# Kernel tuning notes

Hardware: AMD Instinct MI355X
Metric: run time of the kernel (lower is better)

## Reference

```python
import jax, jax.numpy as jnp
import numpy as np

NUM_CLASSES = 40
EOS_COEF = 0.1
IGNORE = 255
W_CLASS, W_MASK, W_DICE = 2.0, 5.0, 5.0
EPS = 1e-8


def setup_inputs() -> dict:
    key = jax.random.key(0)
    k1, k2, k3, k4 = jax.random.split(key, 4)
    B, Q, H, W = 4, 100, 256, 256
    pred_logits = jax.random.normal(k1, (B, Q, NUM_CLASSES + 1), dtype=jnp.float32)
    pred_masks = jax.random.normal(k2, (B, Q, H, W), dtype=jnp.float32)
    targets = jax.random.randint(k3, (B, H, W), 0, NUM_CLASSES)
    ign = jax.random.uniform(k4, (B, H, W)) < 0.05
    targets = jnp.where(ign, IGNORE, targets).astype(jnp.int32)
    return {"pred_logits": pred_logits, "pred_masks": pred_masks, "targets": targets}


def reference(pred_logits, pred_masks, targets):
    B, Q, _ = pred_logits.shape
    C = NUM_CLASSES
    f32 = jnp.float32
    valid = targets != IGNORE                      # [B,H,W]
    tgt_safe = jnp.where(valid, targets, 0)        # in-range for indexing

    # ---- loss_labels: pixel->query assignment, per-query mode label ----
    # sigmoid is monotone, so argmax over queries of raw logits == argmax of sigmoid
    assign = jnp.argmax(pred_masks, axis=1)        # [B,H,W]
    b_idx = jnp.broadcast_to(jnp.arange(B)[:, None, None], targets.shape)
    # counts[b,q,c] = #valid pixels assigned to query q with label c
    counts = jnp.zeros((B, Q, C), f32).at[b_idx, assign, tgt_safe].add(valid.astype(f32))
    has_pix = counts.sum(-1) > 0                   # [B,Q]
    # mode = argmax of counts (ties -> smallest class, matching torch.mode)
    target_classes = jnp.where(has_pix, jnp.argmax(counts, axis=-1), C)  # [B,Q]

    logp = jax.nn.log_softmax(pred_logits, axis=-1)                      # [B,Q,C+1]
    nll = -jnp.take_along_axis(logp, target_classes[..., None], axis=-1)[..., 0]
    empty_weight = jnp.ones(C + 1, f32).at[-1].set(EOS_COEF)
    # ignore_index = num_classes in the CE over classes
    ce = jnp.where(target_classes != C, nll * empty_weight[target_classes], 0.0)
    p = jnp.exp(-ce)
    loss_ce = jnp.mean((1.0 - p) ** 2 * ce)

    # ---- loss_masks: per-pixel CE over queries + per-class dice ----
    logp_pix = jax.nn.log_softmax(pred_masks, axis=1)                    # [B,Q,H,W]
    nll_pix = -jnp.take_along_axis(logp_pix, tgt_safe[:, None], axis=1)[:, 0]  # [B,H,W]
    n_valid = valid.astype(f32).sum()
    ce_mask = jnp.sum(jnp.where(valid, nll_pix, 0.0)) / jnp.maximum(n_valid, 1.0)

    sig = jax.nn.sigmoid(pred_masks)                                     # [B,Q,H,W]
    tmask = (targets[:, None] == jnp.arange(C)[None, :, None, None]).astype(f32)  # [B,C,H,W]
    vm = valid[:, None].astype(f32)                                      # [B,1,H,W]
    inter = jnp.einsum('bqhw,bchw->bqc', sig, tmask * vm)                # numerator uses valid mask
    src_sum = sig.sum(axis=(2, 3))                                       # [B,Q]
    tsum = tmask.sum(axis=(2, 3))                                        # [B,C]
    dice = 2.0 * inter / (src_sum[:, :, None] + tsum[:, None, :] + EPS)  # [B,Q,C]
    present = tsum.sum(axis=0) > 0                                       # [C]
    dice_loss = jnp.sum(jnp.where(present, 1.0 - dice.mean(axis=(0, 1)), 0.0)) / C

    combined = W_MASK * ce_mask + W_DICE * dice_loss
    return W_CLASS * loss_ce + combined
```

## Files before the change

kernel.cpp:

```cpp
#include <hip/hip_runtime.h>
#include <hip/hip_bf16.h>

constexpr int B = 4, Q = 100, C = 40, Cp1 = 41, HW = 65536;
constexpr int NPIX = B * HW;
constexpr int CHUNKS = 4;
constexpr int CPX = HW / CHUNKS;

constexpr int WS_WORDS = 32562;

__global__ void kZ(unsigned* __restrict__ ws, int n) {
    int i = blockIdx.x * blockDim.x + threadIdx.x;
    for (; i < n; i += gridDim.x * blockDim.x) ws[i] = 0u;
}

__global__ __launch_bounds__(256) void kA(const float* __restrict__ masks,
                                          const int* __restrict__ targets,
                                          unsigned* __restrict__ counts,
                                          unsigned* __restrict__ tsum,
                                          float* __restrict__ ce_sum,
                                          unsigned* __restrict__ n_valid) {
    int tid = threadIdx.x;
    int pix = blockIdx.x * 256 + tid;
    int b = pix >> 16;
    int hw = pix & 65535;
    const float* mp = masks + (size_t)b * Q * HW + hw;
    int tgt = targets[pix];

    float m = -INFINITY, s = 0.f, xt = 0.f;
    int amax = 0;
    #pragma unroll 4
    for (int q = 0; q < Q; ++q) {
        float v = mp[(size_t)q * HW];
        float nm = fmaxf(m, v);
        s = s * __expf(m - nm) + __expf(v - nm);
        amax = (v > m) ? q : amax;
        m = nm;
        xt = (q == tgt) ? v : xt;
    }

    __shared__ unsigned ts_local[C];
    __shared__ float cred[4];
    __shared__ unsigned vred[4];
    if (tid < C) ts_local[tid] = 0u;
    __syncthreads();

    float ce = 0.f;
    unsigned nv = 0;
    if (tgt != 255) {
        float lse = m + __logf(s);
        ce = lse - xt;
        nv = 1;
        atomicAdd(&counts[((size_t)b * Q + amax) * C + tgt], 1u);
        atomicAdd(&ts_local[tgt], 1u);
    }

    for (int off = 32; off; off >>= 1) {
        ce += __shfl_xor(ce, off);
        nv += __shfl_xor(nv, off);
    }
    int lane = tid & 63, wave = tid >> 6;
    if (lane == 0) { cred[wave] = ce; vred[wave] = nv; }
    __syncthreads();
    if (tid == 0) {
        atomicAdd(ce_sum, cred[0] + cred[1] + cred[2] + cred[3]);
        atomicAdd(n_valid, vred[0] + vred[1] + vred[2] + vred[3]);
    }
    if (tid < C) {
        unsigned t = ts_local[tid];
        if (t) atomicAdd(&tsum[b * C + tid], t);
    }
}

__global__ __launch_bounds__(256) void kB(const float* __restrict__ masks,
                                          const int* __restrict__ targets,
                                          float* __restrict__ inter,
                                          float* __restrict__ src_sum) {
    __shared__ float hist[C][256];
    int tid = threadIdx.x;
    int bq = blockIdx.x >> 2;
    int chunk = blockIdx.x & 3;
    int b = bq / Q;
    const float* mp = masks + (size_t)bq * HW + chunk * CPX;
    const int* tp = targets + (size_t)b * HW + chunk * CPX;

    #pragma unroll
    for (int c = 0; c < C; ++c) hist[c][tid] = 0.f;

    float sacc = 0.f;
    for (int it = 0; it < CPX / 1024; ++it) {
        int off = it * 1024 + tid * 4;
        float4 x = *(const float4*)(mp + off);
        int4 tg = *(const int4*)(tp + off);
        float xs[4] = {x.x, x.y, x.z, x.w};
        int cs[4] = {tg.x, tg.y, tg.z, tg.w};
        #pragma unroll
        for (int j = 0; j < 4; ++j) {
            float sig = 1.f / (1.f + __expf(-xs[j]));
            sacc += sig;
            if ((unsigned)cs[j] < (unsigned)C) hist[cs[j]][tid] += sig;
        }
    }

    for (int off = 32; off; off >>= 1) sacc += __shfl_xor(sacc, off);
    int lane = tid & 63, wave = tid >> 6;
    if (lane == 0) atomicAdd(&src_sum[bq], sacc);

    __syncthreads();
    for (int c = wave * 10; c < wave * 10 + 10; ++c) {
        float h = hist[c][lane] + hist[c][lane + 64] + hist[c][lane + 128] + hist[c][lane + 192];
        for (int off = 32; off; off >>= 1) h += __shfl_xor(h, off);
        if (lane == 0) atomicAdd(&inter[(size_t)bq * C + c], h);
    }
}

__global__ __launch_bounds__(512) void kC(const float* __restrict__ logits,
                                          const unsigned* __restrict__ counts,
                                          const unsigned* __restrict__ tsum,
                                          const float* __restrict__ inter,
                                          const float* __restrict__ src_sum,
                                          const float* __restrict__ ce_sum,
                                          const unsigned* __restrict__ n_valid,
                                          float* __restrict__ out) {
    int tid = threadIdx.x;
    __shared__ float dice_sum[C];
    __shared__ float wred[8];
    __shared__ float s_lce;
    if (tid < C) dice_sum[tid] = 0.f;

    float ce_acc = 0.f;
    for (int i = tid; i < B * Q; i += 512) {
        const unsigned* cnt = counts + (size_t)i * C;
        unsigned best = 0;
        int tc = C;
        #pragma unroll
        for (int c = 0; c < C; ++c) {
            unsigned v = cnt[c];
            if (v > best) { best = v; tc = c; }
        }
        if (tc != C) {
            const float* lg = logits + (size_t)i * Cp1;
            float mm = -INFINITY, xt = 0.f;
            #pragma unroll
            for (int c = 0; c < Cp1; ++c) {
                float v = lg[c];
                mm = fmaxf(mm, v);
                if (c == tc) xt = v;
            }
            float ss = 0.f;
            #pragma unroll
            for (int c = 0; c < Cp1; ++c) ss += __expf(lg[c] - mm);
            float nll = mm + __logf(ss) - xt;
            float p = __expf(-nll);
            float om = 1.f - p;
            ce_acc += om * om * nll;
        }
    }
    for (int off = 32; off; off >>= 1) ce_acc += __shfl_xor(ce_acc, off);
    if ((tid & 63) == 0) wred[tid >> 6] = ce_acc;
    __syncthreads();
    if (tid == 0) {
        float t = 0.f;
        for (int w = 0; w < 8; ++w) t += wred[w];
        s_lce = t;
    }

    for (int i = tid; i < B * Q * C; i += 512) {
        int bq = i / C, c = i - bq * C;
        float denom = src_sum[bq] + (float)tsum[(bq / Q) * C + c] + 1e-8f;
        atomicAdd(&dice_sum[c], 2.f * inter[i] / denom);
    }
    __syncthreads();

    if (tid == 0) {
        float dl = 0.f;
        for (int c = 0; c < C; ++c) {
            unsigned ts = tsum[c] + tsum[C + c] + tsum[2 * C + c] + tsum[3 * C + c];
            if (ts > 0) dl += 1.f - dice_sum[c] * (1.f / (B * Q));
        }
        dl *= (1.f / C);
        float ce_mask = ce_sum[0] / fmaxf((float)n_valid[0], 1.f);
        float lce = s_lce * (1.f / (B * Q));
        out[0] = 2.f * lce + 5.f * ce_mask + 5.f * dl;
    }
}

extern "C" void kernel_launch(void* const* d_in, const int* in_sizes, int n_in,
                              void* d_out, int out_size, void* d_ws, size_t ws_size,
                              hipStream_t stream) {
    const float* logits  = (const float*)d_in[0];
    const float* masks   = (const float*)d_in[1];
    const int*   targets = (const int*)d_in[2];
    float* out = (float*)d_out;

    unsigned* ws      = (unsigned*)d_ws;
    unsigned* counts  = ws;
    unsigned* tsum    = ws + 16000;
    float*    inter   = (float*)(ws + 16160);
    float*    src_sum = (float*)(ws + 32160);
    float*    ce_sum  = (float*)(ws + 32560);
    unsigned* n_valid = ws + 32561;

    kZ<<<32, 256, 0, stream>>>(ws, WS_WORDS);
    kA<<<NPIX / 256, 256, 0, stream>>>(masks, targets, counts, tsum, ce_sum, n_valid);
    kB<<<B * Q * CHUNKS, 256, 0, stream>>>(masks, targets, inter, src_sum);
    kC<<<1, 512, 0, stream>>>(logits, counts, tsum, inter, src_sum, ce_sum, n_valid, out);
}
```

Before: 239.9 us.

## Fuse mask softmax pass and dice histogram into one read of pred_masks

Merges the per-pixel softmax/argmax kernel with the sigmoid-dice histogram kernel, so the 105MB pred_masks tensor is read once instead of twice. Each thread now handles two pixels with float2 loads. Per-block histograms of sigmoid sums indexed by query and class (plus an ignore bin used for src_sum) are built with shared-memory atomics and written to a scratch buffer. A new reduction kernel then sums them. This adds heavy LDS atomic contention (200 atomics per thread) and about 21MB of scratch writes, traded against halving the main memory traffic.

```diff
diff --git a/kernel.cpp b/kernel.cpp
--- a/kernel.cpp
+++ b/kernel.cpp
@@ -3,57 +3,80 @@
 
 constexpr int B = 4, Q = 100, C = 40, Cp1 = 41, HW = 65536;
 constexpr int NPIX = B * HW;
-constexpr int CHUNKS = 4;
-constexpr int CPX = HW / CHUNKS;
-
-constexpr int WS_WORDS = 32562;
+constexpr int FTHREADS = 256, PXT = 2;
+constexpr int TILE = FTHREADS * PXT;
+constexpr int FBLOCKS = NPIX / TILE;
+constexpr int SLOTS_PER_B = FBLOCKS / B;
+constexpr int HROW = Q * Cp1;
+
+constexpr int ZERO_WORDS = 16162;
 
 __global__ void kZ(unsigned* __restrict__ ws, int n) {
     int i = blockIdx.x * blockDim.x + threadIdx.x;
     for (; i < n; i += gridDim.x * blockDim.x) ws[i] = 0u;
 }
 
-__global__ __launch_bounds__(256) void kA(const float* __restrict__ masks,
+__global__ __launch_bounds__(256) void kF(const float* __restrict__ masks,
                                           const int* __restrict__ targets,
                                           unsigned* __restrict__ counts,
                                           unsigned* __restrict__ tsum,
                                           float* __restrict__ ce_sum,
-                                          unsigned* __restrict__ n_valid) {
-    int tid = threadIdx.x;
-    int pix = blockIdx.x * 256 + tid;
-    int b = pix >> 16;
-    int hw = pix & 65535;
-    const float* mp = masks + (size_t)b * Q * HW + hw;
-    int tgt = targets[pix];
-
-    float m = -INFINITY, s = 0.f, xt = 0.f;
-    int amax = 0;
-    #pragma unroll 4
-    for (int q = 0; q < Q; ++q) {
-        float v = mp[(size_t)q * HW];
-        float nm = fmaxf(m, v);
-        s = s * __expf(m - nm) + __expf(v - nm);
-        amax = (v > m) ? q : amax;
-        m = nm;
-        xt = (q == tgt) ? v : xt;
-    }
-
+                                          unsigned* __restrict__ n_valid,
+                                          float* __restrict__ scratch) {
+    __shared__ float hist[HROW];
     __shared__ unsigned ts_local[C];
     __shared__ float cred[4];
     __shared__ unsigned vred[4];
+
+    int tid = threadIdx.x;
+    int blk = blockIdx.x;
+    int b = blk / SLOTS_PER_B;
+    int hw = (blk % SLOTS_PER_B) * TILE + tid * PXT;
+    const float* mp = masks + (size_t)b * Q * HW + hw;
+    int2 tg = *(const int2*)(targets + (size_t)b * HW + hw);
+    int bin0 = ((unsigned)tg.x < (unsigned)C) ? tg.x : C;
+    int bin1 = ((unsigned)tg.y < (unsigned)C) ? tg.y : C;
+
+    for (int i = tid; i < HROW; i += 256) hist[i] = 0.f;
     if (tid < C) ts_local[tid] = 0u;
     __syncthreads();
+
+    float m0 = -INFINITY, s0 = 0.f, x0 = 0.f;
+    float m1 = -INFINITY, s1 = 0.f, x1 = 0.f;
+    int a0 = 0, a1 = 0;
+    #pragma unroll 4
+    for (int q = 0; q < Q; ++q) {
+        float2 v = *(const float2*)(mp + (size_t)q * HW);
+        float nm0 = fmaxf(m0, v.x);
+        s0 = s0 * __expf(m0 - nm0) + __expf(v.x - nm0);
+        a0 = (v.x > m0) ? q : a0;
+        m0 = nm0;
+        x0 = (q == tg.x) ? v.x : x0;
+        float nm1 = fmaxf(m1, v.y);
+        s1 = s1 * __expf(m1 - nm1) + __expf(v.y - nm1);
+        a1 = (v.y > m1) ? q : a1;
+        m1 = nm1;
+        x1 = (q == tg.y) ? v.y : x1;
+        float sg0 = 1.f / (1.f + __expf(-v.x));
+        float sg1 = 1.f / (1.f + __expf(-v.y));
+        atomicAdd(&hist[q * Cp1 + bin0], sg0);
+        atomicAdd(&hist[q * Cp1 + bin1], sg1);
+    }
 
     float ce = 0.f;
     unsigned nv = 0;
-    if (tgt != 255) {
-        float lse = m + __logf(s);
-        ce = lse - xt;
-        nv = 1;
-        atomicAdd(&counts[((size_t)b * Q + amax) * C + tgt], 1u);
-        atomicAdd(&ts_local[tgt], 1u);
-    }
-
+    if (tg.x != 255) {
+        ce += (m0 + __logf(s0)) - x0;
+        nv++;
+        atomicAdd(&counts[((size_t)b * Q + a0) * C + tg.x], 1u);
+        atomicAdd(&ts_local[tg.x], 1u);
+    }
+    if (tg.y != 255) {
+        ce += (m1 + __logf(s1)) - x1;
+        nv++;
+        atomicAdd(&counts[((size_t)b * Q + a1) * C + tg.y], 1u);
+        atomicAdd(&ts_local[tg.y], 1u);
+    }
     for (int off = 32; off; off >>= 1) {
         ce += __shfl_xor(ce, off);
         nv += __shfl_xor(nv, off);
@@ -61,6 +84,7 @@
     int lane = tid & 63, wave = tid >> 6;
     if (lane == 0) { cred[wave] = ce; vred[wave] = nv; }
     __syncthreads();
+
     if (tid == 0) {
         atomicAdd(ce_sum, cred[0] + cred[1] + cred[2] + cred[3]);
         atomicAdd(n_valid, vred[0] + vred[1] + vred[2] + vred[3]);
@@ -69,47 +93,33 @@
         unsigned t = ts_local[tid];
         if (t) atomicAdd(&tsum[b * C + tid], t);
     }
-}
-
-__global__ __launch_bounds__(256) void kB(const float* __restrict__ masks,
-                                          const int* __restrict__ targets,
+    float* srow = scratch + (size_t)blk * HROW;
+    for (int i = tid; i < HROW; i += 256) srow[i] = hist[i];
+}
+
+__global__ __launch_bounds__(256) void kR(const float* __restrict__ scratch,
                                           float* __restrict__ inter,
                                           float* __restrict__ src_sum) {
-    __shared__ float hist[C][256];
-    int tid = threadIdx.x;
-    int bq = blockIdx.x >> 2;
-    int chunk = blockIdx.x & 3;
-    int b = bq / Q;
-    const float* mp = masks + (size_t)bq * HW + chunk * CPX;
-    const int* tp = targets + (size_t)b * HW + chunk * CPX;
-
-    #pragma unroll
-    for (int c = 0; c < C; ++c) hist[c][tid] = 0.f;
-
-    float sacc = 0.f;
-    for (int it = 0; it < CPX / 1024; ++it) {
-        int off = it * 1024 + tid * 4;
-        float4 x = *(const float4*)(mp + off);
-        int4 tg = *(const int4*)(tp + off);
-        float xs[4] = {x.x, x.y, x.z, x.w};
-        int cs[4] = {tg.x, tg.y, tg.z, tg.w};
-        #pragma unroll
-        for (int j = 0; j < 4; ++j) {
-            float sig = 1.f / (1.f + __expf(-xs[j]));
-            sacc += sig;
-            if ((unsigned)cs[j] < (unsigned)C) hist[cs[j]][tid] += sig;
-        }
-    }
-
-    for (int off = 32; off; off >>= 1) sacc += __shfl_xor(sacc, off);
-    int lane = tid & 63, wave = tid >> 6;
-    if (lane == 0) atomicAdd(&src_sum[bq], sacc);
-
-    __syncthreads();
-    for (int c = wave * 10; c < wave * 10 + 10; ++c) {
-        float h = hist[c][lane] + hist[c][lane + 64] + hist[c][lane + 128] + hist[c][lane + 192];
-        for (int off = 32; off; off >>= 1) h += __shfl_xor(h, off);
-        if (lane == 0) atomicAdd(&inter[(size_t)bq * C + c], h);
+    int bq = blockIdx.x;
+    int b = bq / Q, q = bq - b * Q;
+    int tid = threadIdx.x, w = tid >> 6, c = tid & 63;
+    __shared__ float red[4][64];
+
+    float acc = 0.f;
+    if (c < Cp1) {
+        const float* base = scratch + (size_t)(b * SLOTS_PER_B) * HROW + q * Cp1 + c;
+        #pragma unroll 4
+        for (int i = 0; i < SLOTS_PER_B / 4; ++i)
+            acc += base[(size_t)(w + 4 * i) * HROW];
+    }
+    red[w][c] = acc;
+    __syncthreads();
+    if (tid < 64) {
+        float t = red[0][c] + red[1][c] + red[2][c] + red[3][c];
+        if (c < C) inter[(size_t)bq * C + c] = t;
+        float tt = t;
+        for (int off = 32; off; off >>= 1) tt += __shfl_xor(tt, off);
+        if (c == 0) src_sum[bq] = tt;
     }
 }
 
@@ -195,13 +205,14 @@
     unsigned* ws      = (unsigned*)d_ws;
     unsigned* counts  = ws;
     unsigned* tsum    = ws + 16000;
-    float*    inter   = (float*)(ws + 16160);
-    float*    src_sum = (float*)(ws + 32160);
-    float*    ce_sum  = (float*)(ws + 32560);
-    unsigned* n_valid = ws + 32561;
-
-    kZ<<<32, 256, 0, stream>>>(ws, WS_WORDS);
-    kA<<<NPIX / 256, 256, 0, stream>>>(masks, targets, counts, tsum, ce_sum, n_valid);
-    kB<<<B * Q * CHUNKS, 256, 0, stream>>>(masks, targets, inter, src_sum);
+    float*    ce_sum  = (float*)(ws + 16160);
+    unsigned* n_valid = ws + 16161;
+    float*    inter   = (float*)(ws + 16164);
+    float*    src_sum = (float*)(ws + 32164);
+    float*    scratch = (float*)(ws + 32576);
+
+    kZ<<<64, 256, 0, stream>>>(ws, ZERO_WORDS);
+    kF<<<FBLOCKS, FTHREADS, 0, stream>>>(masks, targets, counts, tsum, ce_sum, n_valid, scratch);
+    kR<<<B * Q, 256, 0, stream>>>(scratch, inter, src_sum);
     kC<<<1, 512, 0, stream>>>(logits, counts, tsum, inter, src_sum, ce_sum, n_valid, out);
 }
```

Measured after the change: 291.1 us. 1.21x slower.
